# Performance work log

Measured on AMD Instinct MI355X. Metric: run time of the kernel, lower is better.

The kernel has to match this reference:

```python
import jax, jax.numpy as jnp
import numpy as np

N_Q = 24
MEAS = (2, 5, 10, 18, 21)


def _build_gates():
    # encoding layer: RY(edge[i]) on wire i
    g = [("ry", "e", i, i) for i in range(N_Q)]
    spec = [
        ("ry", 0, 0), ("ry", 1, 1), ("cx", 0, 1),
        ("ry", 2, 2), ("ry", 3, 3), ("cx", 3, 2),
        ("ry", 4, 4), ("ry", 5, 5), ("cx", 4, 5),
        ("ry", 6, 6), ("ry", 7, 7), ("cx", 7, 6),
        ("ry", 8, 8), ("ry", 9, 9), ("cx", 8, 9),
        ("ry", 10, 10), ("ry", 11, 11), ("cx", 11, 10),
        ("ry", 12, 12), ("ry", 13, 13), ("cx", 12, 13),
        ("ry", 14, 14), ("ry", 15, 15), ("cx", 15, 14),
        ("ry", 16, 16), ("ry", 17, 17), ("cx", 16, 17),
        ("ry", 18, 18), ("ry", 19, 19), ("cx", 19, 18),
        ("ry", 20, 20), ("ry", 21, 21), ("cx", 20, 21),
        ("ry", 22, 22), ("ry", 23, 23), ("cx", 23, 22),
        ("ry", 24, 1), ("ry", 25, 2), ("cx", 1, 2),
        ("ry", 26, 5), ("ry", 27, 6), ("cx", 6, 5),
        ("ry", 28, 9), ("ry", 29, 10), ("cx", 9, 10),
        ("ry", 30, 13), ("ry", 31, 14), ("cx", 14, 13),
        ("ry", 32, 17), ("ry", 33, 18), ("cx", 17, 18),
        ("ry", 34, 21), ("ry", 35, 22), ("cx", 22, 21),
        ("ry", 36, 2), ("ry", 37, 5), ("cx", 2, 5),
        ("ry", 38, 10), ("ry", 39, 13), ("cx", 13, 10),
        ("ry", 40, 18), ("ry", 41, 21), ("cx", 21, 18),
        ("ry", 42, 5), ("ry", 43, 10), ("cx", 5, 10),
        ("ry", 44, 10), ("ry", 45, 18), ("cx", 10, 18),
        ("ry", 46, 5), ("ry", 47, 10), ("cx", 10, 5),
        ("ry", 48, 18), ("ry", 49, 21), ("cx", 18, 21),
        ("ry", 50, 2), ("ry", 51, 5), ("cx", 5, 2),
        ("ry", 52, 2), ("ry", 53, 5), ("ry", 54, 10), ("ry", 55, 18), ("ry", 56, 21),
    ]
    for op in spec:
        if op[0] == "ry":
            g.append(("ry", "t", op[1], op[2]))
        else:
            g.append(("cx", op[1], op[2]))
    return g


GATES = _build_gates()


def _ry(state, ang, w):
    # RY(ang) = [[cos(a/2), -sin(a/2)], [sin(a/2), cos(a/2)]] (real)
    h = 0.5 * ang
    c, s = jnp.cos(h), jnp.sin(h)
    U = jnp.stack([jnp.stack([c, -s]), jnp.stack([s, c])])
    return jnp.moveaxis(jnp.tensordot(U, state, axes=((1,), (w,))), 0, w)


def _cx(state, c, t):
    s = jnp.moveaxis(state, (c, t), (0, 1))
    s = jnp.stack([s[0], s[1][::-1]])  # flip target where control == 1
    return jnp.moveaxis(s, (0, 1), (c, t))


def _expz(state, w):
    p = jnp.moveaxis(state * state, w, 0)
    return jnp.sum(p[0]) - jnp.sum(p[1])


def _run(edge, theta):
    state = jnp.zeros((2,) * N_Q, jnp.float32).at[(0,) * N_Q].set(1.0)
    for g in GATES:
        if g[0] == "ry":
            ang = edge[g[2]] if g[1] == "e" else theta[g[2]]
            state = _ry(state, ang, g[3])
        else:
            state = _cx(state, g[1], g[2])
    return state


def _node_out(edge, theta):
    st = _run(edge, theta)
    ev = jnp.stack([_expz(st, w) for w in MEAS])
    return jnp.pi * (1.0 - ev)  # 2*pi*(1 - ev)/2


def setup_inputs() -> dict:
    key = jax.random.key(0)
    k0, k1, k2, k3, k4 = jax.random.split(key, 5)
    N, E, D = 4, 16, 8
    X = jax.random.uniform(k0, (N, D), jnp.float32)
    e = jax.random.uniform(k1, (E,), jnp.float32)
    Ri = jax.random.uniform(k2, (N, E), jnp.float32)
    Ro = jax.random.uniform(k3, (N, E), jnp.float32)
    theta = jax.random.uniform(k4, (57,), jnp.float32, 0.0, 2.0 * np.pi)
    return {"X": X, "e": e, "Ri": Ri, "Ro": Ro, "theta": theta}


def reference(X, e, Ri, Ro, theta):
    bo = Ro.T @ X                     # [E, D]
    bi = Ri.T @ X                     # [E, D]
    Rwo = Ro * e                      # edge-weighted incidence, e broadcasts over E
    Rwi = Ri * e
    mi = Rwi @ bo                     # [N, D]
    mo = Rwo @ bi                     # [N, D]
    M = jnp.concatenate([mi, mo, X], axis=1)  # [N, 24] angles per node
    return jax.vmap(_node_out, in_axes=(0, None))(M, theta)  # [N, 5]
```

## Files before the change

### kernel.cpp

```cpp
#include <hip/hip_runtime.h>
#include <math.h>


__device__ __forceinline__ void ry_dm(float& a, float& b, float& d, float c, float s) {
    float na = c*c*a - 2.0f*c*s*b + s*s*d;
    float nb = c*s*(a - d) + (c*c - s*s)*b;
    float nd = s*s*a + 2.0f*c*s*b + c*c*d;
    a = na; b = nb; d = nd;
}

template<int MASK>
__device__ __forceinline__ void apply_ry(float* amp, float c, float s) {
#pragma unroll
    for (int i = 0; i < 32; ++i) {
        if (!(i & MASK)) {
            float x = amp[i], y = amp[i | MASK];
            amp[i]        = c * x - s * y;
            amp[i | MASK] = s * x + c * y;
        }
    }
}

template<int MC, int MT>
__device__ __forceinline__ void apply_cx(float* amp) {
#pragma unroll
    for (int i = 0; i < 32; ++i) {
        if ((i & MC) && !(i & MT)) {
            float tmp = amp[i];
            amp[i] = amp[i | MT];
            amp[i | MT] = tmp;
        }
    }
}

__global__ __launch_bounds__(64) void nodenet_branch_kernel(
    const float* __restrict__ X, const float* __restrict__ e,
    const float* __restrict__ Ri, const float* __restrict__ Ro,
    const float* __restrict__ th, float* __restrict__ out)
{
    const int t    = threadIdx.x;
    const int node = blockIdx.x * 2 + (t >> 5);
    const int lig  = t & 31;
    const int base = t & 32;

    float Mv = 0.0f;
    {
        const int w = lig;
        if (w < 8) {
            float acc = 0.0f;
            for (int E = 0; E < 16; ++E) {
                float bo = 0.0f;
                for (int m = 0; m < 4; ++m) bo += Ro[m*16 + E] * X[m*8 + w];
                acc += Ri[node*16 + E] * e[E] * bo;
            }
            Mv = acc;
        } else if (w < 16) {
            const int dcol = w - 8;
            float acc = 0.0f;
            for (int E = 0; E < 16; ++E) {
                float bi = 0.0f;
                for (int m = 0; m < 4; ++m) bi += Ri[m*16 + E] * X[m*8 + dcol];
                acc += Ro[node*16 + E] * e[E] * bi;
            }
            Mv = acc;
        } else {
            Mv = X[node*8 + ((w - 16) & 7)];
        }
    }

    float gs, gc;
    {
        const int id = (lig < 21) ? lig : 0;
        __sincosf(0.5f * th[36 + id], &gs, &gc);
    }

    const int ss = (lig < 6) ? lig : 0;
    const int Q   = ss==0?2 : ss==1?5 : ss==2?10 : ss==3?13 : ss==4?18 : 21;
    const int P   = ss==0?3 : ss==1?4 : ss==2?11 : ss==3?12 : ss==4?19 : 20;
    const int C   = ss==0?1 : ss==1?6 : ss==2?9  : ss==3?14 : ss==4?17 : 22;
    const int PC  = ss==0?0 : ss==1?7 : ss==2?8  : ss==3?15 : ss==4?16 : 23;
    const int tq2 = ss==0?25: ss==1?26: ss==2?29 : ss==3?30 : ss==4?33 : 34;
    const int tc2 = ss==0?24: ss==1?27: ss==2?28 : ss==3?31 : ss==4?32 : 35;

    const float mq  = __shfl(Mv, base + Q);
    const float mp  = __shfl(Mv, base + P);
    const float mc  = __shfl(Mv, base + C);
    const float mpc = __shfl(Mv, base + PC);

    float ra, rb, rd;
    {
        float sq, cq, sp, cp;
        __sincosf(0.5f*(mq + th[Q]), &sq, &cq);
        __sincosf(0.5f*(mp + th[P]), &sp, &cp);
        float aq = cp*cp*cq*cq + sp*sp*sq*sq;
        float bq = cq*sq;
        float dq = 1.0f - aq;

        float sc, cc, spc, cpc;
        __sincosf(0.5f*(mc + th[C]), &sc, &cc);
        __sincosf(0.5f*(mpc + th[PC]), &spc, &cpc);
        float ac = cpc*cpc*cc*cc + spc*spc*sc*sc;
        float bc = cc*sc;
        float dc = 1.0f - ac;

        float s2, c2;
        __sincosf(0.5f*th[tc2], &s2, &c2);
        float p0 = c2*c2*ac - 2.0f*c2*s2*bc + s2*s2*dc;

        float s1, c1;
        __sincosf(0.5f*th[tq2], &s1, &c1);
        ry_dm(aq, bq, dq, c1, s1);
        ra = p0*aq + (1.0f - p0)*dq;
        rb = bq;
        rd = p0*dq + (1.0f - p0)*aq;
    }

    {
        const float c38 = __shfl(gc, base + 2), s38 = __shfl(gs, base + 2);
        const float c39 = __shfl(gc, base + 3), s39 = __shfl(gs, base + 3);
        const float a3 = __shfl(ra, base + 3);
        const float b3 = __shfl(rb, base + 3);
        const float d3 = __shfl(rd, base + 3);
        float a = ra, b = rb, d = rd;
        ry_dm(a, b, d, c38, s38);
        float p0 = c39*c39*a3 - 2.0f*c39*s39*b3 + s39*s39*d3;
        float fa = p0*a + (1.0f - p0)*d;
        float fd = p0*d + (1.0f - p0)*a;
        if (lig == 2) { ra = fa; rb = b; rd = fd; }
    }

    float cph, sph, lam0;
    {
        float ad = ra - rd;
        float r  = sqrtf(ad*ad + 4.0f*rb*rb);
        lam0 = 0.5f * (1.0f + r);
        float c2p = (r > 1e-12f) ? ad / r : 1.0f;
        float s2p = (r > 1e-12f) ? 2.0f*rb / r : 0.0f;
        cph = sqrtf(fmaxf(0.0f, 0.5f*(1.0f + c2p)));
        sph = copysignf(sqrtf(fmaxf(0.0f, 0.5f*(1.0f - c2p))), s2p);
    }

    float u0[5], u1[5];
    float wgt = 1.0f;
    {
        const int slotOf[5] = {0, 1, 2, 4, 5};
#pragma unroll
        for (int b = 0; b < 5; ++b) {
            const float cb = __shfl(cph,  base + slotOf[b]);
            const float sb = __shfl(sph,  base + slotOf[b]);
            const float lb = __shfl(lam0, base + slotOf[b]);
            const int bit = (lig >> b) & 1;
            u0[b] = bit ? -sb : cb;
            u1[b] = bit ?  cb : sb;
            wgt  *= bit ? (1.0f - lb) : lb;
        }
    }

    float c_, s_;
#define BC(id) do { c_ = __shfl(gc, base + (id)); s_ = __shfl(gs, base + (id)); } while (0)

    BC(0); float v00 = c_*u0[0] - s_*u1[0], v01 = s_*u0[0] + c_*u1[0];
    BC(1); float v10 = c_*u0[1] - s_*u1[1], v11 = s_*u0[1] + c_*u1[1];
    float q01_0 = v00*v10, q01_1 = v01*v11, q01_2 = v00*v11, q01_3 = v01*v10;

    BC(4); float v30 = c_*u0[3] - s_*u1[3], v31 = s_*u0[3] + c_*u1[3];
    BC(5); float v40 = c_*u0[4] - s_*u1[4], v41 = s_*u0[4] + c_*u1[4];
    float q34_0 = v30*v40, q34_1 = v31*v40, q34_2 = v31*v41, q34_3 = v30*v41;

    BC(6);
    { float x = q01_0, y = q01_2; q01_0 = c_*x - s_*y; q01_2 = s_*x + c_*y;
      x = q01_1; y = q01_3;       q01_1 = c_*x - s_*y; q01_3 = s_*x + c_*y; }
    BC(7); float v20 = c_*u0[2] - s_*u1[2], v21 = s_*u0[2] + c_*u1[2];
    float q012[8];
    q012[0] = q01_0*v20; q012[1] = q01_1*v20; q012[2] = q01_2*v21; q012[3] = q01_3*v21;
    q012[4] = q01_0*v21; q012[5] = q01_1*v21; q012[6] = q01_2*v20; q012[7] = q01_3*v20;

    BC(8);
#pragma unroll
    for (int j = 0; j < 4; ++j) {
        float x = q012[j], y = q012[j + 4];
        q012[j] = c_*x - s_*y; q012[j + 4] = s_*x + c_*y;
    }
    BC(9);
    { float x = q34_0, y = q34_1; q34_0 = c_*x - s_*y; q34_1 = s_*x + c_*y;
      x = q34_2; y = q34_3;       q34_2 = c_*x - s_*y; q34_3 = s_*x + c_*y; }

    float q34a[4] = {q34_0, q34_1, q34_2, q34_3};
    float amp[32];
#pragma unroll
    for (int j = 0; j < 32; ++j) {
        const int i2 = (j >> 2) & 1, i3 = (j >> 3) & 1, i4 = (j >> 4) & 1;
        amp[j] = q012[j & 7] * q34a[(i3 ^ i2) + 2*i4];
    }

    BC(10); apply_ry<2>(amp, c_, s_);
    BC(11); apply_ry<4>(amp, c_, s_);
    apply_cx<4, 2>(amp);
    BC(12); apply_ry<8>(amp, c_, s_);
    BC(13); apply_ry<16>(amp, c_, s_);
    apply_cx<8, 16>(amp);
    BC(14); apply_ry<1>(amp, c_, s_);
    BC(15); apply_ry<2>(amp, c_, s_);
    apply_cx<2, 1>(amp);
    BC(16); apply_ry<1>(amp, c_, s_);
    BC(17); apply_ry<2>(amp, c_, s_);
    BC(18); apply_ry<4>(amp, c_, s_);
    BC(19); apply_ry<8>(amp, c_, s_);
    BC(20); apply_ry<16>(amp, c_, s_);
#undef BC

    float p[32];
#pragma unroll
    for (int j = 0; j < 32; ++j) p[j] = amp[j] * amp[j];

    float ev0 = 0.f, ev1 = 0.f, ev2 = 0.f, ev3 = 0.f, ev4;
    float s0[16];
#pragma unroll
    for (int i = 0; i < 16; ++i) { s0[i] = p[2*i] + p[2*i+1]; ev0 += p[2*i] - p[2*i+1]; }
    float s1v[8];
#pragma unroll
    for (int i = 0; i < 8; ++i)  { s1v[i] = s0[2*i] + s0[2*i+1]; ev1 += s0[2*i] - s0[2*i+1]; }
    float s2v[4];
#pragma unroll
    for (int i = 0; i < 4; ++i)  { s2v[i] = s1v[2*i] + s1v[2*i+1]; ev2 += s1v[2*i] - s1v[2*i+1]; }
    float s3v[2];
#pragma unroll
    for (int i = 0; i < 2; ++i)  { s3v[i] = s2v[2*i] + s2v[2*i+1]; ev3 += s2v[2*i] - s2v[2*i+1]; }
    ev4 = s3v[0] - s3v[1];

    float ev[5] = {ev0*wgt, ev1*wgt, ev2*wgt, ev3*wgt, ev4*wgt};
#pragma unroll
    for (int off = 1; off < 32; off <<= 1) {
#pragma unroll
        for (int b = 0; b < 5; ++b) ev[b] += __shfl_xor(ev[b], off);
    }

    if (lig < 5) {
        const float v = lig==0 ? ev[0] : lig==1 ? ev[1] : lig==2 ? ev[2]
                      : lig==3 ? ev[3] : ev[4];
        out[node*5 + lig] = 3.14159265358979f * (1.0f - v);
    }
}

extern "C" void kernel_launch(void* const* d_in, const int* in_sizes, int n_in,
                              void* d_out, int out_size, void* d_ws, size_t ws_size,
                              hipStream_t stream) {
    const float* X  = (const float*)d_in[0];
    const float* e  = (const float*)d_in[1];
    const float* Ri = (const float*)d_in[2];
    const float* Ro = (const float*)d_in[3];
    const float* th = (const float*)d_in[4];
    float* out = (float*)d_out;

    nodenet_branch_kernel<<<2, 64, 0, stream>>>(X, e, Ri, Ro, th, out);
}
```

Before: 10.87 us.

## Fold final RY layer into Z/X expectations and pre-apply early RYs on factors

Moves the RY gates 10 and 13 onto the small product-state factors (q012, q34) before the 32-amplitude tensor is built, so they act on 8 or 4 values instead of 32. Drops the last five single-qubit RYs on the full amplitude vector. Their effect is recovered analytically: each final expectation is computed as cos(theta)*<Z> - sin(theta)*<X>, using per-bit <X> correlations taken from the amplitudes. The aim is fewer per-thread FMAs on a tiny, latency-bound kernel. It adds five 16-term correlation sums and relies on the rotated gates commuting with the CX gates that were skipped past them.

```diff
diff --git a/kernel.cpp b/kernel.cpp
--- a/kernel.cpp
+++ b/kernel.cpp
@@ -181,9 +181,19 @@
         float x = q012[j], y = q012[j + 4];
         q012[j] = c_*x - s_*y; q012[j + 4] = s_*x + c_*y;
     }
+    BC(10);
+    { float x, y;
+      x = q012[0]; y = q012[2]; q012[0] = c_*x - s_*y; q012[2] = s_*x + c_*y;
+      x = q012[1]; y = q012[3]; q012[1] = c_*x - s_*y; q012[3] = s_*x + c_*y;
+      x = q012[4]; y = q012[6]; q012[4] = c_*x - s_*y; q012[6] = s_*x + c_*y;
+      x = q012[5]; y = q012[7]; q012[5] = c_*x - s_*y; q012[7] = s_*x + c_*y; }
+
     BC(9);
     { float x = q34_0, y = q34_1; q34_0 = c_*x - s_*y; q34_1 = s_*x + c_*y;
       x = q34_2; y = q34_3;       q34_2 = c_*x - s_*y; q34_3 = s_*x + c_*y; }
+    BC(13);
+    { float x = q34_0, y = q34_2; q34_0 = c_*x - s_*y; q34_2 = s_*x + c_*y;
+      x = q34_1; y = q34_3;       q34_1 = c_*x - s_*y; q34_3 = s_*x + c_*y; }
 
     float q34a[4] = {q34_0, q34_1, q34_2, q34_3};
     float amp[32];
@@ -193,42 +203,53 @@
         amp[j] = q012[j & 7] * q34a[(i3 ^ i2) + 2*i4];
     }
 
-    BC(10); apply_ry<2>(amp, c_, s_);
     BC(11); apply_ry<4>(amp, c_, s_);
     apply_cx<4, 2>(amp);
     BC(12); apply_ry<8>(amp, c_, s_);
-    BC(13); apply_ry<16>(amp, c_, s_);
     apply_cx<8, 16>(amp);
     BC(14); apply_ry<1>(amp, c_, s_);
     BC(15); apply_ry<2>(amp, c_, s_);
     apply_cx<2, 1>(amp);
-    BC(16); apply_ry<1>(amp, c_, s_);
-    BC(17); apply_ry<2>(amp, c_, s_);
-    BC(18); apply_ry<4>(amp, c_, s_);
-    BC(19); apply_ry<8>(amp, c_, s_);
-    BC(20); apply_ry<16>(amp, c_, s_);
+
+    float p[32];
+#pragma unroll
+    for (int j = 0; j < 32; ++j) p[j] = amp[j] * amp[j];
+
+    float z0 = 0.f, z1 = 0.f, z2 = 0.f, z3 = 0.f, z4;
+    float s0[16];
+#pragma unroll
+    for (int i = 0; i < 16; ++i) { s0[i] = p[2*i] + p[2*i+1]; z0 += p[2*i] - p[2*i+1]; }
+    float s1v[8];
+#pragma unroll
+    for (int i = 0; i < 8; ++i)  { s1v[i] = s0[2*i] + s0[2*i+1]; z1 += s0[2*i] - s0[2*i+1]; }
+    float s2v[4];
+#pragma unroll
+    for (int i = 0; i < 4; ++i)  { s2v[i] = s1v[2*i] + s1v[2*i+1]; z2 += s1v[2*i] - s1v[2*i+1]; }
+    float s3v[2];
+#pragma unroll
+    for (int i = 0; i < 2; ++i)  { s3v[i] = s2v[2*i] + s2v[2*i+1]; z3 += s2v[2*i] - s2v[2*i+1]; }
+    z4 = s3v[0] - s3v[1];
+    const float zv[5] = {z0, z1, z2, z3, z4};
+
+    float xv[5];
+#pragma unroll
+    for (int b = 0; b < 5; ++b) {
+        const int m = 1 << b;
+        float acc = 0.0f;
+#pragma unroll
+        for (int i = 0; i < 32; ++i)
+            if (!(i & m)) acc += amp[i] * amp[i | m];
+        xv[b] = 2.0f * acc;
+    }
+
+    float ev[5];
+#pragma unroll
+    for (int b = 0; b < 5; ++b) {
+        BC(16 + b);
+        ev[b] = wgt * ((c_*c_ - s_*s_) * zv[b] - 2.0f*c_*s_ * xv[b]);
+    }
 #undef BC
 
-    float p[32];
-#pragma unroll
-    for (int j = 0; j < 32; ++j) p[j] = amp[j] * amp[j];
-
-    float ev0 = 0.f, ev1 = 0.f, ev2 = 0.f, ev3 = 0.f, ev4;
-    float s0[16];
-#pragma unroll
-    for (int i = 0; i < 16; ++i) { s0[i] = p[2*i] + p[2*i+1]; ev0 += p[2*i] - p[2*i+1]; }
-    float s1v[8];
-#pragma unroll
-    for (int i = 0; i < 8; ++i)  { s1v[i] = s0[2*i] + s0[2*i+1]; ev1 += s0[2*i] - s0[2*i+1]; }
-    float s2v[4];
-#pragma unroll
-    for (int i = 0; i < 4; ++i)  { s2v[i] = s1v[2*i] + s1v[2*i+1]; ev2 += s1v[2*i] - s1v[2*i+1]; }
-    float s3v[2];
-#pragma unroll
-    for (int i = 0; i < 2; ++i)  { s3v[i] = s2v[2*i] + s2v[2*i+1]; ev3 += s2v[2*i] - s2v[2*i+1]; }
-    ev4 = s3v[0] - s3v[1];
-
-    float ev[5] = {ev0*wgt, ev1*wgt, ev2*wgt, ev3*wgt, ev4*wgt};
 #pragma unroll
     for (int off = 1; off < 32; off <<= 1) {
 #pragma unroll
```

Result: faster. 10.45 us (-3.9%).
